# Performance work log

Measured on AMD Instinct MI355X. Metric: run time of the kernel, lower is better.

Reference implementation:

```python
import jax, jax.numpy as jnp
import numpy as np

N = 100000   # nodes
E = 1600000  # edges
D = 128      # state_dim
H1 = 512
H2 = 256


def setup_inputs() -> dict:
    key = jax.random.key(0)
    ks = jax.random.split(key, 8)
    x = jax.random.normal(ks[0], (N, D), jnp.float32)
    edge_index = jax.random.randint(ks[1], (2, E), 0, N, dtype=jnp.int64)
    W_gcn = jax.random.normal(ks[2], (D, D), jnp.float32) * (1.0 / np.sqrt(D))
    b_gcn = jnp.zeros((D,), jnp.float32)
    W1 = jax.random.normal(ks[3], (D, H1), jnp.float32) * (1.0 / np.sqrt(D))
    b1 = jnp.zeros((H1,), jnp.float32)
    W2 = jax.random.normal(ks[4], (H1, H2), jnp.float32) * (1.0 / np.sqrt(H1))
    b2 = jnp.zeros((H2,), jnp.float32)
    W3 = jax.random.normal(ks[5], (H2, 1), jnp.float32) * (1.0 / np.sqrt(H2))
    b3 = jnp.zeros((1,), jnp.float32)
    return {"x": x, "edge_index": edge_index, "W_gcn": W_gcn, "b_gcn": b_gcn,
            "W1": W1, "b1": b1, "W2": W2, "b2": b2, "W3": W3, "b3": b3}


def _gcn_conv(x, edge_index, W, b):
    # PyG GCNConv: linear transform, add self-loops, symmetric deg^-1/2 norm,
    # scatter-sum messages from src to dst, add bias.
    n = x.shape[0]
    loop = jnp.arange(n, dtype=edge_index.dtype)
    src = jnp.concatenate([edge_index[0], loop])
    dst = jnp.concatenate([edge_index[1], loop])
    deg = jax.ops.segment_sum(jnp.ones_like(dst, x.dtype), dst, num_segments=n)
    dinv = jnp.where(deg > 0, jax.lax.rsqrt(jnp.maximum(deg, 1e-12)), 0.0)
    norm = dinv[src] * dinv[dst]                      # [E+N]
    h = x @ W                                         # [N, D]
    msg = h[src] * norm[:, None]                      # gather + scale
    out = jax.ops.segment_sum(msg, dst, num_segments=n)  # scatter-add
    return out + b


def reference(x, edge_index, W_gcn, b_gcn, W1, b1, W2, b2, W3, b3):
    out = jax.nn.relu(_gcn_conv(x, edge_index, W_gcn, b_gcn))
    h = out + x                                       # residual
    h = jax.nn.relu(h @ W1 + b1)
    h = jax.nn.relu(h @ W2 + b2)                      # dropout is identity in eval
    return h @ W3 + b3                                # [N, 1]
```

## Files before the change

### kernel.cpp

```cpp
#include <hip/hip_runtime.h>

#define DN  128
#define H1N 512
#define H2N 256
#define TILE_A 4096
#define BKT_CAP 6144

typedef __attribute__((ext_vector_type(8))) short short8_t;
typedef __attribute__((ext_vector_type(4))) float f32x4;

__device__ inline ushort f2bf(float f) {
  union { float f; unsigned u; } v; v.f = f;
  unsigned r = v.u + 0x7FFF + ((v.u >> 16) & 1);
  return (ushort)(r >> 16);
}
__device__ inline float asf(unsigned u) {
  union { unsigned u; float f; } v; v.u = u;
  return v.f;
}


__global__ __launch_bounds__(256) void k_bucketA(const int* __restrict__ ei,
                                                 int* __restrict__ bcur,
                                                 uint* __restrict__ pairs,
                                                 int E, int NB) {
  __shared__ int hist[512];
  __shared__ int start[512];
  __shared__ int cur[512];
  __shared__ int gbase[512];
  __shared__ uint lp[TILE_A];
  __shared__ ushort bid[TILE_A];
  int t = threadIdx.x;
  int base = blockIdx.x * TILE_A;
  int cnt = E - base; if (cnt > TILE_A) cnt = TILE_A;

  for (int i = t; i < 512; i += 256) hist[i] = 0;
  __syncthreads();

  int sreg[16], dreg[16];
#pragma unroll
  for (int k = 0; k < 16; ++k) {
    int idx = t + 256 * k;
    bool v = idx < cnt;
    sreg[k] = v ? ei[base + idx] : 0;
    dreg[k] = v ? ei[E + base + idx] : -1;
    if (v) atomicAdd(&hist[dreg[k] >> 8], 1);
  }
  __syncthreads();

  for (int i = t; i < 512; i += 256) start[i] = hist[i];
  __syncthreads();
  for (int o = 1; o < 512; o <<= 1) {
    int i0 = t, i1 = t + 256;
    int v0 = (i0 >= o) ? start[i0 - o] : 0;
    int v1 = (i1 >= o) ? start[i1 - o] : 0;
    __syncthreads();
    start[i0] += v0;
    start[i1] += v1;
    __syncthreads();
  }
  for (int i = t; i < 512; i += 256) start[i] -= hist[i];
  __syncthreads();
  for (int i = t; i < 512; i += 256) cur[i] = start[i];
  __syncthreads();

#pragma unroll
  for (int k = 0; k < 16; ++k) {
    if (dreg[k] >= 0) {
      int d = dreg[k] >> 8;
      int p = atomicAdd(&cur[d], 1);
      lp[p]  = ((uint)sreg[k] << 8) | ((uint)dreg[k] & 255u);
      bid[p] = (ushort)d;
    }
  }
  __syncthreads();

  for (int i = t; i < NB; i += 256)
    gbase[i] = hist[i] ? atomicAdd(&bcur[i], hist[i]) : 0;
  __syncthreads();

  for (int p = t; p < cnt; p += 256) {
    int d = bid[p];
    int o = gbase[d] + (p - start[d]);
    if (o < BKT_CAP) pairs[(size_t)d * BKT_CAP + o] = lp[p];
  }
}


__global__ __launch_bounds__(256) void k_bucketB(const uint* __restrict__ pairs,
                                                 const int* __restrict__ bcur,
                                                 int* __restrict__ csr,
                                                 int* __restrict__ ro,
                                                 int* __restrict__ re,
                                                 float* __restrict__ dinv,
                                                 int N) {
  __shared__ int hist[256];
  __shared__ int cur[256];
  __shared__ int lout[BKT_CAP];
  __shared__ uint lp[BKT_CAP];
  int b = blockIdx.x, t = threadIdx.x;
  size_t p0 = (size_t)b * BKT_CAP;
  int cnt = bcur[b]; if (cnt > BKT_CAP) cnt = BKT_CAP;

  hist[t] = 0;
  __syncthreads();
  for (int k = t; k < cnt; k += 256) {
    uint pr = pairs[p0 + k];
    lp[k] = pr;
    atomicAdd(&hist[pr & 255u], 1);
  }
  __syncthreads();

  int v = hist[t];
  cur[t] = v; __syncthreads();
  for (int o = 1; o < 256; o <<= 1) {
    int a = (t >= o) ? cur[t - o] : 0;
    __syncthreads();
    cur[t] += a;
    __syncthreads();
  }
  int excl = cur[t] - v;
  int node = (b << 8) + t;
  if (node < N) {
    ro[node] = (int)p0 + excl;
    re[node] = (int)p0 + excl + v;
    dinv[node] = rsqrtf((float)(v + 1));
  }
  __syncthreads();
  cur[t] = excl;
  __syncthreads();

  for (int k = t; k < cnt; k += 256) {
    uint pr = lp[k];
    int p = atomicAdd(&cur[(int)(pr & 255u)], 1);
    lout[p] = (int)(pr >> 8);
  }
  __syncthreads();
  for (int k = t; k < cnt; k += 256) csr[p0 + k] = lout[k];
}


__device__ inline void pack_one(int idx, const float* __restrict__ W,
                                ushort* __restrict__ Wp, int K, int Ncols) {
  int ksn = K >> 5;
  int l  = idx & 63;
  int ks = (idx >> 6) % ksn;
  int ct = idx / (64 * ksn);
  int col = ct * 16 + (l & 15);
  int kb  = ks * 32 + (l >> 4) * 8;
  short8_t v;
#pragma unroll
  for (int r = 0; r < 8; ++r)
    v[r] = (short)f2bf(W[(size_t)(kb + r) * Ncols + col]);
  *(short8_t*)&Wp[(size_t)idx * 8] = v;
}

__global__ __launch_bounds__(256) void k_packall(const float* __restrict__ Wg,
                                                 const float* __restrict__ W1,
                                                 const float* __restrict__ W2,
                                                 ushort* __restrict__ Wgp,
                                                 ushort* __restrict__ W1p,
                                                 ushort* __restrict__ W2p) {
  int idx = blockIdx.x * 256 + threadIdx.x;
  if (idx < 2048)        pack_one(idx, Wg, Wgp, DN, DN);
  else if (idx < 10240)  pack_one(idx - 2048, W1, W1p, DN, H1N);
  else if (idx < 26624)  pack_one(idx - 10240, W2, W2p, H1N, H2N);
}


__global__ __launch_bounds__(256, 4) void k_gemm1(const float* __restrict__ x,
                                                  const ushort* __restrict__ Wgp,
                                                  const float* __restrict__ dinv,
                                                  ushort* __restrict__ hs,
                                                  ushort* __restrict__ xb, int N) {
  __shared__ ushort xT[64 * 128];
  int t = threadIdx.x;
  int row0 = blockIdx.x * 64;

#pragma unroll
  for (int i = 0; i < 4; ++i) {
    int c = t + 256 * i;
    int r = c >> 4, d0 = (c & 15) * 8;
    int gr = row0 + r;
    float4 v0 = {0,0,0,0}, v1 = {0,0,0,0};
    if (gr < N) {
      v0 = *(const float4*)(x + (size_t)gr * DN + d0);
      v1 = *(const float4*)(x + (size_t)gr * DN + d0 + 4);
    }
    short8_t p;
    p[0]=(short)f2bf(v0.x); p[1]=(short)f2bf(v0.y); p[2]=(short)f2bf(v0.z); p[3]=(short)f2bf(v0.w);
    p[4]=(short)f2bf(v1.x); p[5]=(short)f2bf(v1.y); p[6]=(short)f2bf(v1.z); p[7]=(short)f2bf(v1.w);
    if (gr < N) *(short8_t*)(xb + (size_t)gr * DN + d0) = p;
    *(short8_t*)((char*)xT + r * 256 + ((d0 * 2) ^ ((r & 7) << 4))) = p;
  }
  __syncthreads();

  int w = t >> 6, l = t & 63;
  int lr = l & 15, lk = l >> 4;
  const short8_t* pbg = (const short8_t*)Wgp;

  f32x4 acc[4][2];
#pragma unroll
  for (int mf = 0; mf < 4; ++mf)
#pragma unroll
    for (int n = 0; n < 2; ++n) acc[mf][n] = (f32x4){0.f,0.f,0.f,0.f};

  auto g_load = [&](short8_t (&bb)[2], int ks) {
#pragma unroll
    for (int n = 0; n < 2; ++n)
      bb[n] = pbg[((w * 2 + n) * 4 + ks) * 64 + l];
  };
  auto g_mfma = [&](short8_t (&bb)[2], int ks) {
    short8_t a[4];
#pragma unroll
    for (int mf = 0; mf < 4; ++mf) {
      int r = mf * 16 + lr;
      a[mf] = *(const short8_t*)((const char*)xT + r * 256 + ((ks * 64 + lk * 16) ^ ((r & 7) << 4)));
    }
#pragma unroll
    for (int mf = 0; mf < 4; ++mf)
#pragma unroll
      for (int n = 0; n < 2; ++n)
        acc[mf][n] = __builtin_amdgcn_mfma_f32_16x16x32_bf16(a[mf], bb[n], acc[mf][n], 0, 0, 0);
  };

  short8_t bA[2], bB[2];
  g_load(bA, 0);
  g_load(bB, 1); g_mfma(bA, 0);
  g_load(bA, 2); g_mfma(bB, 1);
  g_load(bB, 3); g_mfma(bA, 2);
  g_mfma(bB, 3);

  float dv[4][4];
#pragma unroll
  for (int mf = 0; mf < 4; ++mf)
#pragma unroll
    for (int r2 = 0; r2 < 4; ++r2) {
      int gr = row0 + mf * 16 + lk * 4 + r2;
      dv[mf][r2] = (gr < N) ? dinv[gr] : 0.f;
    }
#pragma unroll
  for (int n = 0; n < 2; ++n) {
    int col = (w * 2 + n) * 16 + lr;
#pragma unroll
    for (int mf = 0; mf < 4; ++mf)
#pragma unroll
      for (int r2 = 0; r2 < 4; ++r2) {
        int gr = row0 + mf * 16 + lk * 4 + r2;
        if (gr < N) hs[(size_t)gr * DN + col] = f2bf(acc[mf][n][r2] * dv[mf][r2]);
      }
  }
}


__global__ __launch_bounds__(256) void k_agg(const ushort* __restrict__ hs,
                                             const int* __restrict__ csr,
                                             const int* __restrict__ ro,
                                             const int* __restrict__ re,
                                             const float* __restrict__ dinv,
                                             const float* __restrict__ bg,
                                             ushort* __restrict__ aggb, int N) {
  int t = threadIdx.x;
  int node = blockIdx.x * 16 + (t >> 4);
  if (node >= N) return;
  int d0 = (t & 15) * 8;

  int beg = ro[node], end = re[node];
  float dn = dinv[node];
  uint4 selfv = *(const uint4*)(hs + (size_t)node * DN + d0);
  float4 b0 = *(const float4*)(bg + d0);
  float4 b1v = *(const float4*)(bg + d0 + 4);

  float s[8];
#pragma unroll
  for (int i = 0; i < 8; ++i) s[i] = 0.f;

  auto accum = [&](uint4 v) {
    s[0] += asf(v.x << 16); s[1] += asf(v.x & 0xffff0000u);
    s[2] += asf(v.y << 16); s[3] += asf(v.y & 0xffff0000u);
    s[4] += asf(v.z << 16); s[5] += asf(v.z & 0xffff0000u);
    s[6] += asf(v.w << 16); s[7] += asf(v.w & 0xffff0000u);
  };

  int e = beg;
  for (; e + 4 <= end; e += 4) {
    int i0 = csr[e], i1 = csr[e + 1], i2 = csr[e + 2], i3 = csr[e + 3];
    uint4 v0 = *(const uint4*)(hs + (size_t)i0 * DN + d0);
    uint4 v1 = *(const uint4*)(hs + (size_t)i1 * DN + d0);
    uint4 v2 = *(const uint4*)(hs + (size_t)i2 * DN + d0);
    uint4 v3 = *(const uint4*)(hs + (size_t)i3 * DN + d0);
    accum(v0); accum(v1); accum(v2); accum(v3);
  }
  if (e + 2 <= end) {
    int i0 = csr[e], i1 = csr[e + 1];
    uint4 v0 = *(const uint4*)(hs + (size_t)i0 * DN + d0);
    uint4 v1 = *(const uint4*)(hs + (size_t)i1 * DN + d0);
    accum(v0); accum(v1);
    e += 2;
  }
  if (e < end) {
    int i0 = csr[e];
    accum(*(const uint4*)(hs + (size_t)i0 * DN + d0));
  }
  accum(selfv);

  float bv[8] = {b0.x, b0.y, b0.z, b0.w, b1v.x, b1v.y, b1v.z, b1v.w};
  uint outp[4];
#pragma unroll
  for (int i = 0; i < 4; ++i) {
    ushort lo = f2bf(fmaxf(s[2*i]   * dn + bv[2*i],   0.f));
    ushort hi = f2bf(fmaxf(s[2*i+1] * dn + bv[2*i+1], 0.f));
    outp[i] = (uint)lo | ((uint)hi << 16);
  }
  *(uint4*)(aggb + (size_t)node * DN + d0) = *(uint4*)outp;
}


__global__ __launch_bounds__(512, 2) void k_mlp(const ushort* __restrict__ aggb,
                                                const ushort* __restrict__ xb,
                                                const ushort* __restrict__ W1p,
                                                const float* __restrict__ b1,
                                                const ushort* __restrict__ W2p,
                                                const float* __restrict__ b2,
                                                const float* __restrict__ W3,
                                                const float* __restrict__ b3,
                                                float* __restrict__ out, int N) {
  __shared__ ushort aT[64 * 128];
  __shared__ ushort t1[64 * 512];
  int t = threadIdx.x;
  int row0 = blockIdx.x * 64;

#pragma unroll
  for (int i = 0; i < 2; ++i) {
    int c = t + 512 * i;
    int r = c >> 4;
    int d0 = (c & 15) * 8;
    int gr = row0 + r;
    uint4 va = {0, 0, 0, 0}, vx = {0, 0, 0, 0};
    if (gr < N) {
      va = *(const uint4*)(aggb + (size_t)gr * DN + d0);
      vx = *(const uint4*)(xb   + (size_t)gr * DN + d0);
    }
    uint outp[4];
#pragma unroll
    for (int j = 0; j < 4; ++j) {
      uint a = ((const uint*)&va)[j], b = ((const uint*)&vx)[j];
      float lo = asf(a << 16) + asf(b << 16);
      float hi = asf(a & 0xffff0000u) + asf(b & 0xffff0000u);
      outp[j] = (uint)f2bf(lo) | ((uint)f2bf(hi) << 16);
    }
    *(uint4*)((char*)aT + r * 256 + ((d0 * 2) ^ ((r & 7) << 4))) = *(uint4*)outp;
  }
  __syncthreads();

  int w = t >> 6, l = t & 63;
  int lr = l & 15, lk = l >> 4;

  const short8_t* pb1 = (const short8_t*)W1p;
  f32x4 acc1[4][4];
#pragma unroll
  for (int mf = 0; mf < 4; ++mf)
#pragma unroll
    for (int n = 0; n < 4; ++n) acc1[mf][n] = (f32x4){0.f,0.f,0.f,0.f};

  auto s1_load = [&](short8_t (&bb)[4], int ks) {
#pragma unroll
    for (int n = 0; n < 4; ++n)
      bb[n] = pb1[((w * 4 + n) * 4 + ks) * 64 + l];
  };
  auto s1_mfma = [&](short8_t (&bb)[4], int ks) {
    short8_t a[4];
#pragma unroll
    for (int mf = 0; mf < 4; ++mf) {
      int r = mf * 16 + lr;
      a[mf] = *(const short8_t*)((const char*)aT + r * 256 + ((ks * 64 + lk * 16) ^ ((r & 7) << 4)));
    }
#pragma unroll
    for (int mf = 0; mf < 4; ++mf)
#pragma unroll
      for (int n = 0; n < 4; ++n)
        acc1[mf][n] = __builtin_amdgcn_mfma_f32_16x16x32_bf16(a[mf], bb[n], acc1[mf][n], 0, 0, 0);
  };

  {
    short8_t bA[4], bB[4];
    s1_load(bA, 0);
    s1_load(bB, 1); s1_mfma(bA, 0);
    s1_load(bA, 2); s1_mfma(bB, 1);
    s1_load(bB, 3); s1_mfma(bA, 2);
    s1_mfma(bB, 3);
  }

#pragma unroll
  for (int n = 0; n < 4; ++n) {
    int col = (w * 4 + n) * 16 + lr;
    float bb = b1[col];
#pragma unroll
    for (int mf = 0; mf < 4; ++mf)
#pragma unroll
      for (int r2 = 0; r2 < 4; ++r2) {
        int rr = mf * 16 + lk * 4 + r2;
        *(ushort*)((char*)t1 + rr * 1024 + ((col * 2) ^ ((rr & 7) << 4))) =
            f2bf(fmaxf(acc1[mf][n][r2] + bb, 0.f));
      }
  }
  __syncthreads();

  const short8_t* pb2 = (const short8_t*)W2p;
  f32x4 acc2[4][2];
#pragma unroll
  for (int mf = 0; mf < 4; ++mf)
#pragma unroll
    for (int n = 0; n < 2; ++n) acc2[mf][n] = (f32x4){0.f,0.f,0.f,0.f};

  auto s2_load = [&](short8_t (&bb)[4], int p) {
#pragma unroll
    for (int n = 0; n < 2; ++n) {
      bb[n]     = pb2[((w * 2 + n) * 16 + 2 * p)     * 64 + l];
      bb[2 + n] = pb2[((w * 2 + n) * 16 + 2 * p + 1) * 64 + l];
    }
  };
  auto s2_mfma = [&](short8_t (&bb)[4], int p) {
#pragma unroll
    for (int h = 0; h < 2; ++h) {
      int ks = 2 * p + h;
      short8_t a[4];
#pragma unroll
      for (int mf = 0; mf < 4; ++mf) {
        int r = mf * 16 + lr;
        a[mf] = *(const short8_t*)((const char*)t1 + r * 1024 + ((ks * 64 + lk * 16) ^ ((r & 7) << 4)));
      }
#pragma unroll
      for (int mf = 0; mf < 4; ++mf)
#pragma unroll
        for (int n = 0; n < 2; ++n)
          acc2[mf][n] = __builtin_amdgcn_mfma_f32_16x16x32_bf16(a[mf], bb[2 * h + n], acc2[mf][n], 0, 0, 0);
    }
  };

  {
    short8_t c0[4], c1[4], c2[4];
    s2_load(c0, 0); s2_load(c1, 1);
    s2_load(c2, 2); s2_mfma(c0, 0);
    s2_load(c0, 3); s2_mfma(c1, 1);
    s2_load(c1, 4); s2_mfma(c2, 2);
    s2_load(c2, 5); s2_mfma(c0, 3);
    s2_load(c0, 6); s2_mfma(c1, 4);
    s2_load(c1, 7); s2_mfma(c2, 5);
    s2_mfma(c0, 6);
    s2_mfma(c1, 7);
  }

  float po[4][4];
#pragma unroll
  for (int mf = 0; mf < 4; ++mf)
#pragma unroll
    for (int r2 = 0; r2 < 4; ++r2) po[mf][r2] = 0.f;
#pragma unroll
  for (int n = 0; n < 2; ++n) {
    int col = (w * 2 + n) * 16 + lr;
    float bb = b2[col];
    float w3 = W3[col];
#pragma unroll
    for (int mf = 0; mf < 4; ++mf)
#pragma unroll
      for (int r2 = 0; r2 < 4; ++r2)
        po[mf][r2] += fmaxf(acc2[mf][n][r2] + bb, 0.f) * w3;
  }
#pragma unroll
  for (int mf = 0; mf < 4; ++mf)
#pragma unroll
    for (int r2 = 0; r2 < 4; ++r2) {
      float v = po[mf][r2];
      v += __shfl_xor(v, 1, 64);
      v += __shfl_xor(v, 2, 64);
      v += __shfl_xor(v, 4, 64);
      v += __shfl_xor(v, 8, 64);
      po[mf][r2] = v;
    }
  float* pf = (float*)aT;
  if (lr == 0) {
#pragma unroll
    for (int mf = 0; mf < 4; ++mf)
#pragma unroll
      for (int r2 = 0; r2 < 4; ++r2)
        pf[w * 64 + mf * 16 + lk * 4 + r2] = po[mf][r2];
  }
  __syncthreads();
  if (t < 64) {
    int gr = row0 + t;
    if (gr < N) {
      float s = b3[0];
#pragma unroll
      for (int ww = 0; ww < 8; ++ww) s += pf[ww * 64 + t];
      out[gr] = s;
    }
  }
}


extern "C" void kernel_launch(void* const* d_in, const int* in_sizes, int n_in,
                              void* d_out, int out_size, void* d_ws, size_t ws_size,
                              hipStream_t stream) {
  const float* x  = (const float*)d_in[0];
  const int*   ei = (const int*)d_in[1];
  const float* Wg = (const float*)d_in[2];
  const float* bg = (const float*)d_in[3];
  const float* W1 = (const float*)d_in[4];
  const float* b1 = (const float*)d_in[5];
  const float* W2 = (const float*)d_in[6];
  const float* b2 = (const float*)d_in[7];
  const float* W3 = (const float*)d_in[8];
  const float* b3 = (const float*)d_in[9];
  float* out = (float*)d_out;

  const int N = in_sizes[0] / DN;
  const int E = in_sizes[1] / 2;
  const int NB = (N + 255) >> 8;

  char* ws = (char*)d_ws;
  size_t off = 0;
  auto alloc = [&](size_t bytes) -> void* {
    void* p = ws + off;
    off = (off + bytes + 255) & ~(size_t)255;
    return p;
  };
  int*    bcur   = (int*)alloc((size_t)NB * 4);
  int*    ro     = (int*)alloc((size_t)N * 4);
  int*    re     = (int*)alloc((size_t)N * 4);
  float*  dinv   = (float*)alloc((size_t)N * 4);
  int*    csr    = (int*)alloc((size_t)NB * BKT_CAP * 4);
  uint*   pairs  = (uint*)alloc((size_t)NB * BKT_CAP * 4);
  ushort* hsb    = (ushort*)alloc((size_t)N * DN * 2);
  ushort* aggb   = (ushort*)alloc((size_t)N * DN * 2);
  ushort* xbb    = (ushort*)alloc((size_t)N * DN * 2);
  ushort* Wgp    = (ushort*)alloc((size_t)DN * DN * 2);
  ushort* W1p    = (ushort*)alloc((size_t)DN * H1N * 2);
  ushort* W2p    = (ushort*)alloc((size_t)H1N * H2N * 2);
  (void)ws_size; (void)n_in; (void)out_size;

  hipMemsetAsync(bcur, 0, (size_t)NB * 4, stream);

  int nTiles = (E + TILE_A - 1) / TILE_A;
  k_bucketA<<<nTiles, 256, 0, stream>>>(ei, bcur, pairs, E, NB);
  k_bucketB<<<NB, 256, 0, stream>>>(pairs, bcur, csr, ro, re, dinv, N);

  k_packall<<<104, 256, 0, stream>>>(Wg, W1, W2, Wgp, W1p, W2p);

  int nb64 = (N + 63) / 64;
  k_gemm1<<<nb64, 256, 0, stream>>>(x, Wgp, dinv, hsb, xbb, N);
  k_agg<<<(N + 15) / 16, 256, 0, stream>>>(hsb, csr, ro, re, dinv, bg, aggb, N);
  k_mlp<<<nb64, 512, 0, stream>>>(aggb, xbb, W1p, b1, W2p, b2, W3, b3, out, N);
}
```

Baseline: 193.2 us.

## Slice feature layout into 16-column panels for cache-local gather and fuse residual

Stores hs, xb and agg in a column-sliced layout of 8 slices × N × 16 bf16, and launches the aggregation with the slice index in the fastest-varying block bits. Blocks running at the same time then gather from one 3.2MB slice that can stay in L2/LLC, instead of from the full 25.6MB feature table. The residual add of x moves from the MLP kernel into the aggregation epilogue, so the MLP loads a single input stream. In exchange, each gather fetches only 32 bytes per row, and the CSR indices are read eight times, once per slice.

```diff
diff --git a/kernel.cpp b/kernel.cpp
--- a/kernel.cpp
+++ b/kernel.cpp
@@ -190,7 +190,10 @@
     short8_t p;
     p[0]=(short)f2bf(v0.x); p[1]=(short)f2bf(v0.y); p[2]=(short)f2bf(v0.z); p[3]=(short)f2bf(v0.w);
     p[4]=(short)f2bf(v1.x); p[5]=(short)f2bf(v1.y); p[6]=(short)f2bf(v1.z); p[7]=(short)f2bf(v1.w);
-    if (gr < N) *(short8_t*)(xb + (size_t)gr * DN + d0) = p;
+    if (gr < N) {
+      int s = (c & 15) >> 1, half = (c & 15) & 1;
+      *(short8_t*)(xb + ((size_t)s * N + gr) * 16 + half * 8) = p;
+    }
     *(short8_t*)((char*)xT + r * 256 + ((d0 * 2) ^ ((r & 7) << 4))) = p;
   }
   __syncthreads();
@@ -241,19 +244,21 @@
     }
 #pragma unroll
   for (int n = 0; n < 2; ++n) {
-    int col = (w * 2 + n) * 16 + lr;
+    int s = w * 2 + n;
 #pragma unroll
     for (int mf = 0; mf < 4; ++mf)
 #pragma unroll
       for (int r2 = 0; r2 < 4; ++r2) {
         int gr = row0 + mf * 16 + lk * 4 + r2;
-        if (gr < N) hs[(size_t)gr * DN + col] = f2bf(acc[mf][n][r2] * dv[mf][r2]);
+        if (gr < N)
+          hs[((size_t)s * N + gr) * 16 + lr] = f2bf(acc[mf][n][r2] * dv[mf][r2]);
       }
   }
 }
 
 
 __global__ __launch_bounds__(256) void k_agg(const ushort* __restrict__ hs,
+                                             const ushort* __restrict__ xb,
                                              const int* __restrict__ csr,
                                              const int* __restrict__ ro,
                                              const int* __restrict__ re,
@@ -261,63 +266,60 @@
                                              const float* __restrict__ bg,
                                              ushort* __restrict__ aggb, int N) {
   int t = threadIdx.x;
-  int node = blockIdx.x * 16 + (t >> 4);
+  int slice = blockIdx.x & 7;
+  int node = (blockIdx.x >> 3) * 64 + (t >> 2);
   if (node >= N) return;
-  int d0 = (t & 15) * 8;
-
+  int d0 = (t & 3) * 4;
+
+  const ushort* hss = hs + (size_t)slice * N * 16;
   int beg = ro[node], end = re[node];
   float dn = dinv[node];
-  uint4 selfv = *(const uint4*)(hs + (size_t)node * DN + d0);
-  float4 b0 = *(const float4*)(bg + d0);
-  float4 b1v = *(const float4*)(bg + d0 + 4);
-
-  float s[8];
-#pragma unroll
-  for (int i = 0; i < 8; ++i) s[i] = 0.f;
-
-  auto accum = [&](uint4 v) {
-    s[0] += asf(v.x << 16); s[1] += asf(v.x & 0xffff0000u);
-    s[2] += asf(v.y << 16); s[3] += asf(v.y & 0xffff0000u);
-    s[4] += asf(v.z << 16); s[5] += asf(v.z & 0xffff0000u);
-    s[6] += asf(v.w << 16); s[7] += asf(v.w & 0xffff0000u);
+  uint2 selfv = *(const uint2*)(hss + (size_t)node * 16 + d0);
+  uint2 xv    = *(const uint2*)(xb + ((size_t)slice * N + node) * 16 + d0);
+  float4 bv   = *(const float4*)(bg + slice * 16 + d0);
+
+  float s0 = 0.f, s1 = 0.f, s2 = 0.f, s3 = 0.f;
+  auto accum = [&](uint2 v) {
+    s0 += asf(v.x << 16); s1 += asf(v.x & 0xffff0000u);
+    s2 += asf(v.y << 16); s3 += asf(v.y & 0xffff0000u);
   };
 
   int e = beg;
   for (; e + 4 <= end; e += 4) {
     int i0 = csr[e], i1 = csr[e + 1], i2 = csr[e + 2], i3 = csr[e + 3];
-    uint4 v0 = *(const uint4*)(hs + (size_t)i0 * DN + d0);
-    uint4 v1 = *(const uint4*)(hs + (size_t)i1 * DN + d0);
-    uint4 v2 = *(const uint4*)(hs + (size_t)i2 * DN + d0);
-    uint4 v3 = *(const uint4*)(hs + (size_t)i3 * DN + d0);
+    uint2 v0 = *(const uint2*)(hss + (size_t)i0 * 16 + d0);
+    uint2 v1 = *(const uint2*)(hss + (size_t)i1 * 16 + d0);
+    uint2 v2 = *(const uint2*)(hss + (size_t)i2 * 16 + d0);
+    uint2 v3 = *(const uint2*)(hss + (size_t)i3 * 16 + d0);
     accum(v0); accum(v1); accum(v2); accum(v3);
   }
   if (e + 2 <= end) {
     int i0 = csr[e], i1 = csr[e + 1];
-    uint4 v0 = *(const uint4*)(hs + (size_t)i0 * DN + d0);
-    uint4 v1 = *(const uint4*)(hs + (size_t)i1 * DN + d0);
+    uint2 v0 = *(const uint2*)(hss + (size_t)i0 * 16 + d0);
+    uint2 v1 = *(const uint2*)(hss + (size_t)i1 * 16 + d0);
     accum(v0); accum(v1);
     e += 2;
   }
   if (e < end) {
     int i0 = csr[e];
-    accum(*(const uint4*)(hs + (size_t)i0 * DN + d0));
+    accum(*(const uint2*)(hss + (size_t)i0 * 16 + d0));
   }
   accum(selfv);
 
-  float bv[8] = {b0.x, b0.y, b0.z, b0.w, b1v.x, b1v.y, b1v.z, b1v.w};
-  uint outp[4];
-#pragma unroll
-  for (int i = 0; i < 4; ++i) {
-    ushort lo = f2bf(fmaxf(s[2*i]   * dn + bv[2*i],   0.f));
-    ushort hi = f2bf(fmaxf(s[2*i+1] * dn + bv[2*i+1], 0.f));
-    outp[i] = (uint)lo | ((uint)hi << 16);
-  }
-  *(uint4*)(aggb + (size_t)node * DN + d0) = *(uint4*)outp;
+  uint outp[2];
+  {
+    ushort lo = f2bf(fmaxf(s0 * dn + bv.x, 0.f) + asf(xv.x << 16));
+    ushort hi = f2bf(fmaxf(s1 * dn + bv.y, 0.f) + asf(xv.x & 0xffff0000u));
+    outp[0] = (uint)lo | ((uint)hi << 16);
+    lo = f2bf(fmaxf(s2 * dn + bv.z, 0.f) + asf(xv.y << 16));
+    hi = f2bf(fmaxf(s3 * dn + bv.w, 0.f) + asf(xv.y & 0xffff0000u));
+    outp[1] = (uint)lo | ((uint)hi << 16);
+  }
+  *(uint2*)(aggb + ((size_t)slice * N + node) * 16 + d0) = *(uint2*)outp;
 }
 
 
 __global__ __launch_bounds__(512, 2) void k_mlp(const ushort* __restrict__ aggb,
-                                                const ushort* __restrict__ xb,
                                                 const ushort* __restrict__ W1p,
                                                 const float* __restrict__ b1,
                                                 const ushort* __restrict__ W2p,
@@ -332,24 +334,15 @@
 
 #pragma unroll
   for (int i = 0; i < 2; ++i) {
-    int c = t + 512 * i;
-    int r = c >> 4;
-    int d0 = (c & 15) * 8;
+    int u = t + 512 * i;
+    int slice = u >> 7;
+    int v = u & 127;
+    int r = v >> 1, half = v & 1;
     int gr = row0 + r;
-    uint4 va = {0, 0, 0, 0}, vx = {0, 0, 0, 0};
-    if (gr < N) {
-      va = *(const uint4*)(aggb + (size_t)gr * DN + d0);
-      vx = *(const uint4*)(xb   + (size_t)gr * DN + d0);
-    }
-    uint outp[4];
-#pragma unroll
-    for (int j = 0; j < 4; ++j) {
-      uint a = ((const uint*)&va)[j], b = ((const uint*)&vx)[j];
-      float lo = asf(a << 16) + asf(b << 16);
-      float hi = asf(a & 0xffff0000u) + asf(b & 0xffff0000u);
-      outp[j] = (uint)f2bf(lo) | ((uint)f2bf(hi) << 16);
-    }
-    *(uint4*)((char*)aT + r * 256 + ((d0 * 2) ^ ((r & 7) << 4))) = *(uint4*)outp;
+    uint4 val = {0, 0, 0, 0};
+    if (gr < N) val = *(const uint4*)(aggb + ((size_t)slice * N + gr) * 16 + half * 8);
+    int d0 = slice * 16 + half * 8;
+    *(uint4*)((char*)aT + r * 256 + ((d0 * 2) ^ ((r & 7) << 4))) = val;
   }
   __syncthreads();
 
@@ -549,6 +542,6 @@
 
   int nb64 = (N + 63) / 64;
   k_gemm1<<<nb64, 256, 0, stream>>>(x, Wgp, dinv, hsb, xbb, N);
-  k_agg<<<(N + 15) / 16, 256, 0, stream>>>(hsb, csr, ro, re, dinv, bg, aggb, N);
-  k_mlp<<<nb64, 512, 0, stream>>>(aggb, xbb, W1p, b1, W2p, b2, W3, b3, out, N);
-}
+  k_agg<<<nb64 * 8, 256, 0, stream>>>(hsb, xbb, csr, ro, re, dinv, bg, aggb, N);
+  k_mlp<<<nb64, 512, 0, stream>>>(aggb, W1p, b1, W2p, b2, W3, b3, out, N);
+}
```

Result: slower. 214.1 us (+10.8%).
